# Performance work log

Measured on AMD Instinct MI355X. Metric: run time of the kernel, lower is better.

The kernel has to match this reference:

```python
import jax, jax.numpy as jnp
import numpy as np

N_ENT = 50000
N_REL = 500
DIM = 256
BATCH = 512
EPS = 1e-5


def setup_inputs() -> dict:
    key = jax.random.key(0)
    ks = jax.random.split(key, 5)
    E_emb = jax.random.normal(ks[0], (4, N_ENT, DIM), jnp.float32)   # (a_re, a_im, b_re, b_im)
    R_emb = jax.random.normal(ks[1], (4, N_REL, DIM), jnp.float32)
    psi_emb = jax.random.normal(ks[2], (N_REL, DIM), jnp.float32)
    bn_gamma = jnp.ones((4, DIM), jnp.float32)
    bn_beta = jnp.zeros((4, DIM), jnp.float32)
    biases = jnp.zeros((4, N_ENT), jnp.float32)                      # b_a, b_x, b_y, b_z
    h_idx = jax.random.randint(ks[3], (BATCH,), 0, N_ENT)
    r_idx = jax.random.randint(ks[4], (BATCH,), 0, N_REL)
    return dict(E_emb=E_emb, R_emb=R_emb, psi_emb=psi_emb, bn_gamma=bn_gamma,
                bn_beta=bn_beta, biases=biases, h_idx=h_idx, r_idx=r_idx)


def _qnorm(q):
    # QubitNorm: normalize so |a|^2 + |b|^2 = 1 per embedding coordinate.
    # q: [4, ..., d] stacked real parts.
    length = jnp.sqrt(jnp.sum(q * q, axis=0, keepdims=True))
    return q / length


def _bn(q, gamma, beta):
    # QubitBatchNorm1d (training-mode batch stats), per component and per feature.
    # q: [4, B, d]
    mean = q.mean(axis=1, keepdims=True)
    var = q.var(axis=1, keepdims=True)
    return (q - mean) / jnp.sqrt(var + EPS) * gamma[:, None, :] + beta[:, None, :]


def _cmul(a, b):
    return (a[0] * b[0] - a[1] * b[1], a[0] * b[1] + a[1] * b[0])


def reference(E_emb, R_emb, psi_emb, bn_gamma, bn_beta, biases, h_idx, r_idx):
    # h = E_bn(norm(E(h_idx)))
    h = _bn(_qnorm(E_emb[:, h_idx]), bn_gamma, bn_beta)   # [4, B, d]
    # r = norm(R(r_idx))
    r = _qnorm(R_emb[:, r_idx])                           # [4, B, d]
    psi = psi_emb[r_idx]                                  # [B, d]
    z = (jnp.cos(psi), jnp.sin(psi))
    h_a, h_b = (h[0], h[1]), (h[2], h[3])
    r_a, r_b = (r[0], r[1]), (r[2], r[3])
    ra_conj = (r[0], -r[1])
    rb_conj = (r[2], -r[3])
    # QubitMult: a = h_a*r_a - z*(h_b*conj(r_b)); b = h_a*r_b + z*(h_b*conj(r_a))
    m1 = _cmul(h_a, r_a)
    m2 = _cmul(z, _cmul(h_b, rb_conj))
    m3 = _cmul(h_a, r_b)
    m4 = _cmul(z, _cmul(h_b, ra_conj))
    t = jnp.stack([m1[0] - m2[0], m1[1] - m2[1], m3[0] + m4[0], m3[1] + m4[1]])  # [4, B, d]
    # All-entity table: E_bn(norm(E))
    E = _bn(_qnorm(E_emb), bn_gamma, bn_beta)             # [4, N, d]
    # QubitScoringAll: per-component dot product against all entities (dropout = eval identity)
    scores = jnp.einsum('cbd,cnd->cbn', t, E)             # [4, B, N]
    y = jax.nn.sigmoid(scores + biases[:, None, :])       # (y_a, y_ai, y_b, y_bi) stacked
    return y
```

## Files before the change

kernel.cpp:

```cpp
#include <hip/hip_runtime.h>
#include <math.h>

#define NENT 50000
#define NREL 500
#define DIM 256
#define BATCH 512
#define EPSV 1e-5f

#define WS_ACC    0
#define WS_KC     8192
#define WS_F16    10240

typedef _Float16 f16x8 __attribute__((ext_vector_type(8)));
typedef _Float16 f16x4 __attribute__((ext_vector_type(4)));
typedef float f32x4 __attribute__((ext_vector_type(4)));
typedef float f32x16 __attribute__((ext_vector_type(16)));

__device__ inline f32x16 zero16() {
    f32x16 v;
#pragma unroll
    for (int i = 0; i < 16; ++i) v[i] = 0.f;
    return v;
}

__global__ void convert_stats_kernel(const float* __restrict__ E, _Float16* __restrict__ Eh,
                                     float* __restrict__ acc, const int* __restrict__ h_idx) {
    if (blockIdx.x >= 512) {
        int d = threadIdx.x;
        int b0 = (blockIdx.x - 512) * 32;
        float sm0=0,sm1=0,sm2=0,sm3=0, sq0=0,sq1=0,sq2=0,sq3=0;
        for (int j = 0; j < 32; ++j) {
            int n = h_idx[b0 + j];
            int ga = n*DIM + d;
            float e0 = E[ga];
            float e1 = E[1*NENT*DIM + ga];
            float e2 = E[2*NENT*DIM + ga];
            float e3 = E[3*NENT*DIM + ga];
            float inv = rsqrtf(e0*e0+e1*e1+e2*e2+e3*e3);
            e0*=inv; e1*=inv; e2*=inv; e3*=inv;
            sm0+=e0; sq0+=e0*e0;
            sm1+=e1; sq1+=e1*e1;
            sm2+=e2; sq2+=e2*e2;
            sm3+=e3; sq3+=e3*e3;
        }
        atomicAdd(&acc[2048 + 0*DIM+d], sm0); atomicAdd(&acc[3072 + 0*DIM+d], sq0);
        atomicAdd(&acc[2048 + 1*DIM+d], sm1); atomicAdd(&acc[3072 + 1*DIM+d], sq1);
        atomicAdd(&acc[2048 + 2*DIM+d], sm2); atomicAdd(&acc[3072 + 2*DIM+d], sq2);
        atomicAdd(&acc[2048 + 3*DIM+d], sm3); atomicAdd(&acc[3072 + 3*DIM+d], sq3);
        return;
    }

    __shared__ float red[3][64][33];
    int tid = threadIdx.x;
    int dq = tid & 63, j = tid >> 6;
    int d0 = dq * 4;
    int per = (NENT + 511) / 512;
    int n0 = blockIdx.x * per;
    int n1 = n0 + per; if (n1 > NENT) n1 = NENT;

    float sm[4][4]; float sq[4][4];
#pragma unroll
    for (int c = 0; c < 4; ++c)
#pragma unroll
        for (int dd = 0; dd < 4; ++dd) { sm[c][dd] = 0.f; sq[c][dd] = 0.f; }

    for (int n = n0 + j; n < n1; n += 4) {
        size_t ga = (size_t)n * DIM + d0;
        f32x4 e[4];
        e[0] = *(const f32x4*)(E + ga);
        e[1] = *(const f32x4*)(E + (size_t)NENT * DIM + ga);
        e[2] = *(const f32x4*)(E + (size_t)2 * NENT * DIM + ga);
        e[3] = *(const f32x4*)(E + (size_t)3 * NENT * DIM + ga);
        float inv[4];
#pragma unroll
        for (int dd = 0; dd < 4; ++dd)
            inv[dd] = rsqrtf(e[0][dd]*e[0][dd] + e[1][dd]*e[1][dd] +
                             e[2][dd]*e[2][dd] + e[3][dd]*e[3][dd]);
#pragma unroll
        for (int c = 0; c < 4; ++c) {
            f16x4 hv;
#pragma unroll
            for (int dd = 0; dd < 4; ++dd) {
                float v = e[c][dd] * inv[dd];
                hv[dd] = (_Float16)v;
                sm[c][dd] += v; sq[c][dd] += v * v;
            }
            __builtin_nontemporal_store(hv, (f16x4*)(Eh + (size_t)c * NENT * DIM + ga));
        }
    }

    if (j > 0) {
        float* p = &red[j-1][dq][0];
#pragma unroll
        for (int c = 0; c < 4; ++c)
#pragma unroll
            for (int dd = 0; dd < 4; ++dd) {
                p[c*4 + dd]      = sm[c][dd];
                p[16 + c*4 + dd] = sq[c][dd];
            }
    }
    __syncthreads();
    if (j == 0) {
#pragma unroll
        for (int c = 0; c < 4; ++c)
#pragma unroll
            for (int dd = 0; dd < 4; ++dd) {
                float s = sm[c][dd] + red[0][dq][c*4+dd] + red[1][dq][c*4+dd] + red[2][dq][c*4+dd];
                float q = sq[c][dd] + red[0][dq][16+c*4+dd] + red[1][dq][16+c*4+dd] + red[2][dq][16+c*4+dd];
                atomicAdd(&acc[c*DIM + d0 + dd], s);
                atomicAdd(&acc[1024 + c*DIM + d0 + dd], q);
            }
    }
}

__global__ void build_t_kernel(const float* __restrict__ E, const float* __restrict__ R,
                               const float* __restrict__ psi_emb,
                               const float* __restrict__ gamma, const float* __restrict__ beta,
                               const int* __restrict__ h_idx, const int* __restrict__ r_idx,
                               const float* __restrict__ acc,
                               _Float16* __restrict__ th, float* __restrict__ Kc) {
    __shared__ float red[4];
    int b = blockIdx.x, d = threadIdx.x;
    int wave = d >> 6, lane = d & 63;
    int hn = h_idx[b], rn = r_idx[b];

    float mE[4], isE[4], mH[4], isH[4];
#pragma unroll
    for (int c = 0; c < 4; ++c) {
        float a0 = acc[c*DIM + d];
        float a1 = acc[1024 + c*DIM + d];
        float a2 = acc[2048 + c*DIM + d];
        float a3 = acc[3072 + c*DIM + d];
        mE[c] = a0 * (1.0f / NENT);
        float vE = a1 * (1.0f / NENT) - mE[c] * mE[c];
        isE[c] = rsqrtf(vE + EPSV);
        mH[c] = a2 * (1.0f / BATCH);
        float vH = a3 * (1.0f / BATCH) - mH[c] * mH[c];
        isH[c] = rsqrtf(vH + EPSV);
    }

    float hv[4];
    hv[0] = E[hn*DIM + d];
    hv[1] = E[1*NENT*DIM + hn*DIM + d];
    hv[2] = E[2*NENT*DIM + hn*DIM + d];
    hv[3] = E[3*NENT*DIM + hn*DIM + d];
    float invh = rsqrtf(hv[0]*hv[0]+hv[1]*hv[1]+hv[2]*hv[2]+hv[3]*hv[3]);
    float hq[4];
#pragma unroll
    for (int c = 0; c < 4; ++c) {
        float v = hv[c] * invh;
        hq[c] = (v - mH[c]) * isH[c] * gamma[c*DIM + d] + beta[c*DIM + d];
    }

    float r0 = R[rn*DIM + d];
    float r1 = R[1*NREL*DIM + rn*DIM + d];
    float r2 = R[2*NREL*DIM + rn*DIM + d];
    float r3 = R[3*NREL*DIM + rn*DIM + d];
    float invr = rsqrtf(r0*r0+r1*r1+r2*r2+r3*r3);
    r0*=invr; r1*=invr; r2*=invr; r3*=invr;

    float p = psi_emb[rn*DIM + d];
    float cz = cosf(p), sz = sinf(p);

    float m1r = hq[0]*r0 - hq[1]*r1;
    float m1i = hq[0]*r1 + hq[1]*r0;
    float X   = hq[2]*r2 + hq[3]*r3;
    float Y   = hq[3]*r2 - hq[2]*r3;
    float m2r = cz*X - sz*Y;
    float m2i = cz*Y + sz*X;
    float m3r = hq[0]*r2 - hq[1]*r3;
    float m3i = hq[0]*r3 + hq[1]*r2;
    float U   = hq[2]*r0 + hq[3]*r1;
    float V   = hq[3]*r0 - hq[2]*r1;
    float m4r = cz*U - sz*V;
    float m4i = cz*V + sz*U;

    float t[4] = { m1r - m2r, m1i - m2i, m3r + m4r, m3i + m4i };

#pragma unroll
    for (int c = 0; c < 4; ++c) {
        float g   = gamma[c*DIM + d];
        th[((size_t)c*BATCH + b)*DIM + d] = (_Float16)(t[c] * g * isE[c]);
        float kp = t[c] * (beta[c*DIM + d] - g * mE[c] * isE[c]);
#pragma unroll
        for (int off = 32; off > 0; off >>= 1) kp += __shfl_down(kp, off, 64);
        if (lane == 0) red[wave] = kp;
        __syncthreads();
        if (d == 0) Kc[c*BATCH + b] = red[0] + red[1] + red[2] + red[3];
        __syncthreads();
    }
}

__launch_bounds__(256)
__global__ void score_gemm_kernel(const _Float16* __restrict__ th,
                                  const _Float16* __restrict__ Eh,
                                  const float* __restrict__ Kc,
                                  const float* __restrict__ biases,
                                  float* __restrict__ out) {
    __shared__ __align__(1024) char smem[32768 + 512];
    int tid = threadIdx.x;
    int w = tid >> 6, l = tid & 63;
    int lr = l & 31, lh = l >> 5;
    int wm = w & 1, wn = w >> 1;

    int lin = blockIdx.x + (int)gridDim.x * (blockIdx.y + (int)gridDim.y * blockIdx.z);
    int wg  = (lin & 7) * 782 + (lin >> 3);
    int bt  = wg & 3;
    int nt  = (wg >> 2) % 391;
    int c   = wg / 1564;
    int b0  = bt * 128;
    int n0  = nt * 128;

    const _Float16* Ah = th + (size_t)c * BATCH * DIM;
    const _Float16* Bh = Eh + (size_t)c * NENT * DIM;
    const float* Kcc = Kc + c * BATCH;
    const float* bc  = biases + (size_t)c * NENT;

    int ng0 = n0 + wn*64 + lr;
    int ng1 = ng0 + 32;
    int ng0c = ng0 > NENT-1 ? NENT-1 : ng0;
    int ng1c = ng1 > NENT-1 ? NENT-1 : ng1;
    float bv0 = bc[ng0c];
    float bv1 = bc[ng1c];
    if (w < 2) {
        __builtin_amdgcn_global_load_lds(
            (const __attribute__((address_space(1))) void*)(Kcc + b0 + w*64 + l),
            (__attribute__((address_space(3))) void*)(smem + 32768 + w*256),
            4, 0, 0);
    }
    float* kcs = (float*)(smem + 32768);

    f32x16 acc00 = zero16(), acc01 = zero16(), acc10 = zero16(), acc11 = zero16();

    auto stage = [&](int kc, int slot) {
        int kbase = kc * 32;
#pragma unroll
        for (int i = 0; i < 4; ++i) {
            int f = w * 4 + i;
            const _Float16* gp;
            if (f < 8) {
                int mf = f >> 1, ks = f & 1;
                gp = Ah + (size_t)(b0 + mf*32 + lr) * DIM + kbase + ks*16 + lh*8;
            } else {
                int g = f - 8, nf = g >> 1, ks = g & 1;
                int n = n0 + nf*32 + lr; if (n > NENT-1) n = NENT-1;
                gp = Bh + (size_t)n * DIM + kbase + ks*16 + lh*8;
            }
            __builtin_amdgcn_global_load_lds(
                (const __attribute__((address_space(1))) void*)gp,
                (__attribute__((address_space(3))) void*)(smem + slot * 16384 + f * 1024),
                16, 0, 0);
        }
    };

    auto compute = [&](int slot) {
        const char* s = smem + slot * 16384;
#pragma unroll
        for (int ks = 0; ks < 2; ++ks) {
            f16x8 a0  = *(const f16x8*)(s + ((wm*2+0)*2 + ks)*1024 + l*16);
            f16x8 a1  = *(const f16x8*)(s + ((wm*2+1)*2 + ks)*1024 + l*16);
            f16x8 bb0 = *(const f16x8*)(s + 8192 + ((wn*2+0)*2 + ks)*1024 + l*16);
            f16x8 bb1 = *(const f16x8*)(s + 8192 + ((wn*2+1)*2 + ks)*1024 + l*16);
            acc00 = __builtin_amdgcn_mfma_f32_32x32x16_f16(a0, bb0, acc00, 0, 0, 0);
            acc01 = __builtin_amdgcn_mfma_f32_32x32x16_f16(a0, bb1, acc01, 0, 0, 0);
            acc10 = __builtin_amdgcn_mfma_f32_32x32x16_f16(a1, bb0, acc10, 0, 0, 0);
            acc11 = __builtin_amdgcn_mfma_f32_32x32x16_f16(a1, bb1, acc11, 0, 0, 0);
        }
    };

    stage(0, 0);
    for (int t = 0; t < 7; ++t) {
        stage(t + 1, (t + 1) & 1);
        asm volatile("s_waitcnt vmcnt(4)" ::: "memory");
        __builtin_amdgcn_s_barrier();
        compute(t & 1);
        __builtin_amdgcn_s_barrier();
    }
    asm volatile("s_waitcnt vmcnt(0)" ::: "memory");
    __builtin_amdgcn_s_barrier();
    compute(1);

    float* oc = out + (size_t)c * BATCH * NENT;
#pragma unroll
    for (int mi = 0; mi < 2; ++mi) {
#pragma unroll
        for (int ni = 0; ni < 2; ++ni) {
            const f32x16& a = (mi==0) ? (ni==0 ? acc00 : acc01) : (ni==0 ? acc10 : acc11);
            int n = ni == 0 ? ng0 : ng1;
            bool ok = (n < NENT);
            float bv = ni == 0 ? bv0 : bv1;
#pragma unroll
            for (int reg = 0; reg < 16; ++reg) {
                int mloc = wm*64 + mi*32 + (reg & 3) + 8*(reg >> 2) + 4*lh;
                float x = a[reg] + kcs[mloc] + bv;
                float y = 1.f / (1.f + __expf(-x));
                if (ok) __builtin_nontemporal_store(y, &oc[(size_t)(b0 + mloc) * NENT + n]);
            }
        }
    }
}

extern "C" void kernel_launch(void* const* d_in, const int* in_sizes, int n_in,
                              void* d_out, int out_size, void* d_ws, size_t ws_size,
                              hipStream_t stream) {
    const float* E      = (const float*)d_in[0];
    const float* R      = (const float*)d_in[1];
    const float* psi    = (const float*)d_in[2];
    const float* gamma  = (const float*)d_in[3];
    const float* beta   = (const float*)d_in[4];
    const float* biases = (const float*)d_in[5];
    const int* h_idx    = (const int*)d_in[6];
    const int* r_idx    = (const int*)d_in[7];
    float* out = (float*)d_out;
    float* ws  = (float*)d_ws;

    _Float16* th = (_Float16*)(ws + WS_F16);
    _Float16* Eh = th + (size_t)4 * BATCH * DIM;

    hipMemsetAsync(ws + WS_ACC, 0, 4096 * sizeof(float), stream);

    convert_stats_kernel<<<528, 256, 0, stream>>>(E, Eh, ws + WS_ACC, h_idx);
    build_t_kernel<<<BATCH, 256, 0, stream>>>(E, R, psi, gamma, beta, h_idx, r_idx,
                                              ws + WS_ACC, th, ws + WS_KC);
    dim3 grid((NENT + 127) / 128, BATCH / 128, 4);
    score_gemm_kernel<<<grid, 256, 0, stream>>>(th, Eh, ws + WS_KC, biases, out);
}
```

Measured before the change: 769.5 us.

## Triple-buffer score GEMM LDS pipeline and batch Kc reductions in build_t

The score GEMM goes from a two-slot to a three-slot LDS ring, prefetching two K-chunks ahead with adjusted vmcnt waits so global loads overlap further with MFMA compute. This raises LDS use per block from 32KB to 48KB, which can lower occupancy. Separately, build_t now reduces all four Kc components in one shuffle pass with a single barrier instead of four reductions with eight barriers. The build_t change is a small kernel and matters little next to the GEMM, which is output-write heavy.

```diff
diff --git a/kernel.cpp b/kernel.cpp
--- a/kernel.cpp
+++ b/kernel.cpp
@@ -119,7 +119,7 @@
                                const int* __restrict__ h_idx, const int* __restrict__ r_idx,
                                const float* __restrict__ acc,
                                _Float16* __restrict__ th, float* __restrict__ Kc) {
-    __shared__ float red[4];
+    __shared__ float red[16];
     int b = blockIdx.x, d = threadIdx.x;
     int wave = d >> 6, lane = d & 63;
     int hn = h_idx[b], rn = r_idx[b];
@@ -177,18 +177,25 @@
 
     float t[4] = { m1r - m2r, m1i - m2i, m3r + m4r, m3i + m4i };
 
+    float kp[4];
 #pragma unroll
     for (int c = 0; c < 4; ++c) {
-        float g   = gamma[c*DIM + d];
+        float g = gamma[c*DIM + d];
         th[((size_t)c*BATCH + b)*DIM + d] = (_Float16)(t[c] * g * isE[c]);
-        float kp = t[c] * (beta[c*DIM + d] - g * mE[c] * isE[c]);
-#pragma unroll
-        for (int off = 32; off > 0; off >>= 1) kp += __shfl_down(kp, off, 64);
-        if (lane == 0) red[wave] = kp;
-        __syncthreads();
-        if (d == 0) Kc[c*BATCH + b] = red[0] + red[1] + red[2] + red[3];
-        __syncthreads();
-    }
+        kp[c] = t[c] * (beta[c*DIM + d] - g * mE[c] * isE[c]);
+    }
+#pragma unroll
+    for (int off = 32; off > 0; off >>= 1) {
+#pragma unroll
+        for (int c = 0; c < 4; ++c) kp[c] += __shfl_down(kp[c], off, 64);
+    }
+    if (lane == 0) {
+#pragma unroll
+        for (int c = 0; c < 4; ++c) red[wave*4 + c] = kp[c];
+    }
+    __syncthreads();
+    if (d < 4)
+        Kc[d*BATCH + b] = red[0*4+d] + red[1*4+d] + red[2*4+d] + red[3*4+d];
 }
 
 __launch_bounds__(256)
@@ -197,7 +204,7 @@
                                   const float* __restrict__ Kc,
                                   const float* __restrict__ biases,
                                   float* __restrict__ out) {
-    __shared__ __align__(1024) char smem[32768 + 512];
+    __shared__ __align__(1024) char smem[49152 + 512];
     int tid = threadIdx.x;
     int w = tid >> 6, l = tid & 63;
     int lr = l & 31, lh = l >> 5;
@@ -225,10 +232,10 @@
     if (w < 2) {
         __builtin_amdgcn_global_load_lds(
             (const __attribute__((address_space(1))) void*)(Kcc + b0 + w*64 + l),
-            (__attribute__((address_space(3))) void*)(smem + 32768 + w*256),
+            (__attribute__((address_space(3))) void*)(smem + 49152 + w*256),
             4, 0, 0);
     }
-    float* kcs = (float*)(smem + 32768);
+    float* kcs = (float*)(smem + 49152);
 
     f32x16 acc00 = zero16(), acc01 = zero16(), acc10 = zero16(), acc11 = zero16();
 
@@ -269,16 +276,21 @@
     };
 
     stage(0, 0);
-    for (int t = 0; t < 7; ++t) {
-        stage(t + 1, (t + 1) & 1);
-        asm volatile("s_waitcnt vmcnt(4)" ::: "memory");
+    stage(1, 1);
+#pragma unroll 1
+    for (int t = 0; t < 8; ++t) {
+        if (t < 6) {
+            stage(t + 2, (t + 2) % 3);
+            asm volatile("s_waitcnt vmcnt(8)" ::: "memory");
+        } else if (t == 6) {
+            asm volatile("s_waitcnt vmcnt(4)" ::: "memory");
+        } else {
+            asm volatile("s_waitcnt vmcnt(0)" ::: "memory");
+        }
         __builtin_amdgcn_s_barrier();
-        compute(t & 1);
+        compute(t % 3);
         __builtin_amdgcn_s_barrier();
     }
-    asm volatile("s_waitcnt vmcnt(0)" ::: "memory");
-    __builtin_amdgcn_s_barrier();
-    compute(1);
 
     float* oc = out + (size_t)c * BATCH * NENT;
 #pragma unroll
```

Result: no change. 765.4 us (-0.5%).
